# Kernel optimization log

Hardware: AMD Instinct MI355X
Metric: run time of the kernel (lower is better)

Reference implementation:

```python
import jax, jax.numpy as jnp
import numpy as np

B, N, E, P, PH, H = 4, 512, 768, 64, 32, 8
D = E // H  # 96
FFN = 3072

def _ln(x, g, b, eps=1e-5):
    mu = jnp.mean(x, axis=-1, keepdims=True)
    var = jnp.mean((x - mu) ** 2, axis=-1, keepdims=True)
    return (x - mu) * jax.lax.rsqrt(var + eps) * g + b

def setup_inputs() -> dict:
    key = jax.random.key(0)
    ks = iter(jax.random.split(key, 80))
    def f(*s):
        return jax.random.normal(next(ks), s, jnp.float32) * 0.02
    ones = lambda *s: jnp.ones(s, jnp.float32)
    zeros = lambda *s: jnp.zeros(s, jnp.float32)
    return {
        'x': jax.random.normal(next(ks), (B, N, E), jnp.float32),
        'pair': jax.random.normal(next(ks), (B, N, N, P), jnp.float32) * 0.5,
        'attn_mask': zeros(B, 1, N, N),
        'op_mask': ones(B, N, 1),
        'op_norm': ones(1) / N,
        'nlist': jax.random.randint(next(ks), (B, N, 64), 0, N),
        'wq': f(E, E), 'wk': f(E, E), 'wv': f(E, E),
        'wg': f(E, E), 'bg': zeros(E),
        'wo': f(E, E), 'bo': zeros(E),
        'ln_pair_g': ones(P), 'ln_pair_b': zeros(P),
        'wb': f(H, P), 'bb': zeros(H),
        'ln_attn_g': ones(E), 'ln_attn_b': zeros(E),
        'ln_ffn_g': ones(E), 'ln_ffn_b': zeros(E),
        'w_ffn1': f(FFN, E), 'b_ffn1': zeros(FFN),
        'w_ffn2': f(E, FFN), 'b_ffn2': zeros(E),
        'ln_opm_g': ones(E), 'ln_opm_b': zeros(E),
        'w_opm_in': f(2 * PH, E), 'b_opm_in': zeros(2 * PH),
        'w_opm_out': f(P, PH * PH), 'b_opm_out': zeros(P),
        'ln_tm_g': ones(P), 'ln_tm_b': zeros(P),
        'w_tm_abp': f(2 * PH, P), 'b_tm_abp': zeros(2 * PH),
        'w_tm_abg': f(2 * PH, P), 'b_tm_abg': zeros(2 * PH),
        'w_tm_g': f(P, P), 'b_tm_g': zeros(P),
        'w_tm_z': f(P, PH), 'b_tm_z': zeros(P),
        'ln_tmo_g': ones(PH), 'ln_tmo_b': zeros(PH),
        'ln_pffn_g': ones(P), 'ln_pffn_b': zeros(P),
        'w_pffn1': f(P, P), 'b_pffn1': zeros(P),
        'w_pffn2': f(P, P), 'b_pffn2': zeros(P),
    }

def _forward(x, pair, attn_mask, op_mask, op_norm, wq, wk, wv, wg, bg, wo, bo,
             ln_pair_g, ln_pair_b, wb, bb, ln_attn_g, ln_attn_b,
             ln_ffn_g, ln_ffn_b, w_ffn1, b_ffn1, w_ffn2, b_ffn2,
             ln_opm_g, ln_opm_b, w_opm_in, b_opm_in, w_opm_out, b_opm_out,
             ln_tm_g, ln_tm_b, w_tm_abp, b_tm_abp, w_tm_abg, b_tm_abg,
             w_tm_g, b_tm_g, w_tm_z, b_tm_z, ln_tmo_g, ln_tmo_b,
             ln_pffn_g, ln_pffn_b, w_pffn1, b_pffn1, w_pffn2, b_pffn2):
    Bx, Nx, _ = x.shape
    # --- gated pair-bias self-attention (pre-LN, eval mode: dropout = identity) ---
    h = _ln(x, ln_attn_g, ln_attn_b)
    pn = _ln(pair, ln_pair_g, ln_pair_b)               # AtomAttention pair LayerNorm
    bias = jnp.einsum('bijp,hp->bhij', pn, wb) + bb[None, :, None, None]
    q = (h @ wq.T).reshape(Bx, Nx, H, D).transpose(0, 2, 1, 3) * (D ** -0.5)
    k = (h @ wk.T).reshape(Bx, Nx, H, D).transpose(0, 2, 1, 3)
    v = (h @ wv.T).reshape(Bx, Nx, H, D).transpose(0, 2, 1, 3)
    attn = jax.nn.softmax(jnp.einsum('bhid,bhjd->bhij', q, k) + attn_mask + bias, axis=-1)
    o = jnp.einsum('bhij,bhjd->bhid', attn, v).transpose(0, 2, 1, 3).reshape(Bx, Nx, E)
    o = jax.nn.sigmoid(h @ wg.T + bg) * o              # sigmoid output gate
    x = x + (o @ wo.T + bo)
    # --- atom transition MLP ---
    h = _ln(x, ln_ffn_g, ln_ffn_b)
    x = x + (jax.nn.gelu(h @ w_ffn1.T + b_ffn1, approximate=False) @ w_ffn2.T + b_ffn2)
    # --- OuterProduct pair update (fused: avoids [B,N,N,PH*PH] intermediate) ---
    h = _ln(x, ln_opm_g, ln_opm_b)
    ab = (h @ w_opm_in.T + b_opm_in) * op_mask
    a_o, b_o = jnp.split(ab, 2, axis=-1)               # each [B,N,PH]
    z = jnp.einsum('bid,bje,pde->bijp', a_o, b_o, w_opm_out.reshape(P, PH, PH)) + b_opm_out
    pair = pair + z * op_norm
    # --- triangle multiplication ---
    zp = _ln(pair, ln_tm_g, ln_tm_b)
    gpr = zp @ w_tm_g.T + b_tm_g                       # gate (no sigmoid, matches source)
    ab = (zp @ w_tm_abp.T + b_tm_abp) * jax.nn.sigmoid(zp @ w_tm_abg.T + b_tm_abg)
    a_t, b_t = jnp.split(ab, 2, axis=-1)               # each [B,N,N,PH]
    t = jnp.einsum('bijh,bkjh->bhik', a_t, b_t) + jnp.einsum('bjih,bjkh->bhik', a_t, b_t)
    t = _ln(t.transpose(0, 2, 3, 1), ln_tmo_g, ln_tmo_b) @ w_tm_z.T + b_tm_z
    pair = pair + gpr * t
    # --- pair transition MLP ---
    zp = _ln(pair, ln_pffn_g, ln_pffn_b)
    pair = pair + (jax.nn.gelu(zp @ w_pffn1.T + b_pffn1, approximate=False) @ w_pffn2.T + b_pffn2)
    return x, pair

def reference(x, pair, attn_mask, op_mask, op_norm, nlist, wq, wk, wv, wg, bg, wo, bo,
              ln_pair_g, ln_pair_b, wb, bb, ln_attn_g, ln_attn_b,
              ln_ffn_g, ln_ffn_b, w_ffn1, b_ffn1, w_ffn2, b_ffn2,
              ln_opm_g, ln_opm_b, w_opm_in, b_opm_in, w_opm_out, b_opm_out,
              ln_tm_g, ln_tm_b, w_tm_abp, b_tm_abp, w_tm_abg, b_tm_abg,
              w_tm_g, b_tm_g, w_tm_z, b_tm_z, ln_tmo_g, ln_tmo_b,
              ln_pffn_g, ln_pffn_b, w_pffn1, b_pffn1, w_pffn2, b_pffn2):
    del nlist  # accepted by the torch module but unused in the math
    return _forward(x, pair, attn_mask, op_mask, op_norm, wq, wk, wv, wg, bg, wo, bo,
                    ln_pair_g, ln_pair_b, wb, bb, ln_attn_g, ln_attn_b,
                    ln_ffn_g, ln_ffn_b, w_ffn1, b_ffn1, w_ffn2, b_ffn2,
                    ln_opm_g, ln_opm_b, w_opm_in, b_opm_in, w_opm_out, b_opm_out,
                    ln_tm_g, ln_tm_b, w_tm_abp, b_tm_abp, w_tm_abg, b_tm_abg,
                    w_tm_g, b_tm_g, w_tm_z, b_tm_z, ln_tmo_g, ln_tmo_b,
                    ln_pffn_g, ln_pffn_b, w_pffn1, b_pffn1, w_pffn2, b_pffn2)
```

## Files before the change

### kernel.cpp

```cpp
#include <hip/hip_runtime.h>
#include <hip/hip_bf16.h>
#include <math.h>

#define Nn 512
#define Ee 768
#define Pp 64
#define PHh 32
#define Hh 8
#define Dd 96
#define NNe 262144
#define LNEPS 1e-5f

typedef __attribute__((ext_vector_type(8))) short bf8;
typedef __attribute__((ext_vector_type(4))) short bf4;
typedef __attribute__((ext_vector_type(4))) float f32x4;
#define MFMA(a,b,c) __builtin_amdgcn_mfma_f32_16x16x32_bf16(a,b,c,0,0,0)

__device__ __forceinline__ short f2bf(float f) {
  unsigned u = __builtin_bit_cast(unsigned, f);
  unsigned r = (u + 0x7fffu + ((u >> 16) & 1u)) >> 16;
  return (short)r;
}
__device__ __forceinline__ float bf2f(short s) {
  unsigned u = ((unsigned)(unsigned short)s) << 16;
// ... 376 lines not shown
  float rsum[4] = {0.f, 0.f, 0.f, 0.f};
#pragma unroll
  for (int jf = 0; jf < 8; ++jf)
#pragma unroll
    for (int r = 0; r < 4; ++r) {
      float e = __expf(sv[jf][r] - rmax[r]);
      sv[jf][r] = e;
      rsum[r] += e;
    }
#pragma unroll
  for (int r = 0; r < 4; ++r) {
#pragma unroll
    for (int off = 1; off < 16; off <<= 1) rsum[r] += __shfl_xor(rsum[r], off, 16);
    if (llo == 0) redB[wv][lhi * 4 + r] = rsum[r];
  }
  __syncthreads();
#pragma unroll
  for (int r = 0; r < 4; ++r) {
    int row = lhi * 4 + r;
    float s = redB[0][row] + redB[1][row] + redB[2][row] + redB[3][row];
    float inv = 1.f / s;
#pragma unroll
    for (int jf = 0; jf < 8; ++jf) {
      int j = jb0 + jf * 16 + llo;
      out_bf[bioff + (long)row * 512 + j] = f2bf(sv[jf][r] * inv);
    }
  }
}

__global__ __launch_bounds__(256) void opm_T_kernel(const float* __restrict__ ab,
                                                    const float* __restrict__ mask,
                                                    const float* __restrict__ w,
                                                    short* __restrict__ T,
                                                    short* __restrict__ bo_bf) {
  int p = blockIdx.y;
  int row = blockIdx.x * 8 + threadIdx.y;
  int e = threadIdx.x;
  float mk = mask[row];
  const float* a = ab + (long)row * 64;
  const float* wp = w + p * 1024 + e;
  float acc = 0.f;
#pragma unroll
  for (int d = 0; d < 32; ++d) acc += a[d] * wp[d * 32];
  T[((long)row * 64 + p) * 32 + e] = f2bf(acc * mk);
  if (blockIdx.y == 0) bo_bf[(long)row * 32 + e] = f2bf(a[32 + e] * mk);
}

__global__ __launch_bounds__(256) void pair_bias_mfma(
    const float* __restrict__ pair, const float* __restrict__ gam,
    const float* __restrict__ bet, const short* __restrict__ wb_a,
    const float* __restrict__ bbv, short* __restrict__ bias,
    short* __restrict__ pair_bf) {
  __shared__ __align__(16) short Zb[64 * 72];
  __shared__ __align__(16) short Wb[16 * 72];
  __shared__ float sp[4][2][72];
  int tid = threadIdx.x;
  long e0 = (long)blockIdx.x * 64;
  int b = (int)(e0 >> 18);
  long ein = e0 & (NNe - 1);
  const float* base = pair + e0 * 64;
  for (int l = tid; l < 1024; l += 256) {
    int h = l >> 6, c = l & 63;
    Wb[h * 72 + c] = (h < 8) ? wb_a[h * 64 + c] : (short)0;
  }
  int e = tid & 63, q = tid >> 6;
  f32x4 v4[4];
  float s = 0.f, ss = 0.f;
#pragma unroll
  for (int k = 0; k < 4; ++k) {
    v4[k] = *(const f32x4*)(base + (long)e * 64 + q * 16 + k * 4);
#pragma unroll
    for (int u = 0; u < 4; ++u) { float v = v4[k][u]; s += v; ss += v * v; }
  }
#pragma unroll
  for (int k = 0; k < 4; ++k) {
    bf4 pr;
#pragma unroll
    for (int u = 0; u < 4; ++u) pr[u] = f2bf(v4[k][u]);
    *(bf4*)(pair_bf + (e0 + e) * 64 + q * 16 + k * 4) = pr;
  }
  sp[q][0][e] = s; sp[q][1][e] = ss;
  __syncthreads();
  float ts = sp[0][0][e] + sp[1][0][e] + sp[2][0][e] + sp[3][0][e];
  float tss = sp[0][1][e] + sp[1][1][e] + sp[2][1][e] + sp[3][1][e];
  float mu = ts * 0.015625f, var = tss * 0.015625f - mu * mu;
  float rs = rsqrtf(var + LNEPS);
#pragma unroll
  for (int k = 0; k < 4; ++k) {
    bf4 pk;
#pragma unroll
    for (int u = 0; u < 4; ++u) {
      int c = q * 16 + k * 4 + u;
      pk[u] = f2bf((v4[k][u] - mu) * rs * gam[c] + bet[c]);
    }
    *(bf4*)&Zb[e * 72 + q * 16 + k * 4] = pk;
  }
  __syncthreads();
  int wv = tid >> 6, lane = tid & 63;
  int lhi = lane >> 4, llo = lane & 15;
  int n0 = wv * 16;
  f32x4 acc = {0.f, 0.f, 0.f, 0.f};
#pragma unroll
  for (int ks = 0; ks < 2; ++ks) {
    bf8 a = *(const bf8*)&Wb[llo * 72 + ks * 32 + lhi * 8];
    bf8 bz = *(const bf8*)&Zb[(n0 + llo) * 72 + ks * 32 + lhi * 8];
    acc = MFMA(a, bz, acc);
  }
  int elem = n0 + llo;
#pragma unroll
  for (int r = 0; r < 4; ++r) {
    int h = lhi * 4 + r;
    if (h < 8) bias[(long)(b * 8 + h) * NNe + ein + elem] = f2bf(acc[r] + bbv[h]);
  }
}

__global__ __launch_bounds__(256) void opm_ab_fused(
    const short* __restrict__ pair_bf, const short* __restrict__ Tb,
    const short* __restrict__ bo_bf, const float* __restrict__ b_out,
    const float* __restrict__ op_norm, const float* __restrict__ gam,
    const float* __restrict__ bet, const short* __restrict__ wp_a,
    const float* __restrict__ b_abp, const short* __restrict__ wg_a,
    const float* __restrict__ b_abg,
    short* __restrict__ aN4, short* __restrict__ bN4) {
  int jt = blockIdx.x;
  int i = blockIdx.y;
  int bb = blockIdx.z;
  int tid = threadIdx.x;
  __shared__ __align__(16) short Tsb[64 * 40];
  __shared__ __align__(16) short Bob[64 * 40];
  __shared__ __align__(16) short Zb[64 * 72];
  __shared__ __align__(16) short Wp[64 * 72];
  __shared__ __align__(16) short Wg[64 * 72];
  __shared__ float spS[64][9];
  __shared__ float spQ[64][9];
  int wv = tid >> 6, lane = tid & 63;
  int wr = wv >> 1, wc = wv & 1;
  int lhi = lane >> 4, llo = lane & 15;
  int chb = wr * 32 + lhi * 4;
  long grow = (long)bb * 512 + i;
  {
    int p = tid >> 2, e8 = (tid & 3) * 8;
    *(bf8*)&Tsb[p * 40 + e8] = *(const bf8*)(Tb + grow * 2048 + p * 32 + e8);
    *(bf8*)&Bob[p * 40 + e8] =
        *(const bf8*)(bo_bf + ((long)bb * 512 + jt * 64 + p) * 32 + e8);
  }
  for (int l = tid; l < 512; l += 256) {
    int r = l >> 3, c8 = (l & 7) * 8;
    *(bf8*)&Wp[r * 72 + c8] = *(const bf8*)(wp_a + r * 64 + c8);
    *(bf8*)&Wg[r * 72 + c8] = *(const bf8*)(wg_a + r * 64 + c8);
  }
  long ebase = (long)i * 512 + jt * 64;
  const short* pbase = pair_bf + ((long)bb * NNe + ebase) * 64;
  short* aN = aN4 + (long)bb * 8388608;
  short* bN = bN4 + (long)bb * 8388608;
  f32x4 x[2][2];
#pragma unroll
  for (int mi = 0; mi < 2; ++mi)
#pragma unroll
    for (int ni = 0; ni < 2; ++ni) {
      bf4 pv = *(const bf4*)(pbase + (long)(wc * 32 + ni * 16 + llo) * 64 +
                             chb + mi * 16);
#pragma unroll
      for (int r = 0; r < 4; ++r) x[mi][ni][r] = bf2f(pv[r]);
    }
  __syncthreads();
  f32x4 acc[2][2] = {};
  {
    bf8 a0 = *(const bf8*)&Tsb[(wr * 32 + llo) * 40 + lhi * 8];
    bf8 a1 = *(const bf8*)&Tsb[(wr * 32 + 16 + llo) * 40 + lhi * 8];
    bf8 b0 = *(const bf8*)&Bob[(wc * 32 + llo) * 40 + lhi * 8];
    bf8 b1 = *(const bf8*)&Bob[(wc * 32 + 16 + llo) * 40 + lhi * 8];
    acc[0][0] = MFMA(a0, b0, acc[0][0]);
    acc[0][1] = MFMA(a0, b1, acc[0][1]);
    acc[1][0] = MFMA(a1, b0, acc[1][0]);
    acc[1][1] = MFMA(a1, b1, acc[1][1]);
  }
  float nrm = op_norm[0];
#pragma unroll
  for (int mi = 0; mi < 2; ++mi) {
    f32x4 bo4 = *(const f32x4*)(b_out + chb + mi * 16);
#pragma unroll
    for (int ni = 0; ni < 2; ++ni)
#pragma unroll
      for (int r = 0; r < 4; ++r)
        x[mi][ni][r] += (acc[mi][ni][r] + bo4[r]) * nrm;
  }
#pragma unroll
  for (int ni = 0; ni < 2; ++ni) {
    float s = 0.f, ss = 0.f;
#pragma unroll
    for (int mi = 0; mi < 2; ++mi)
#pragma unroll
      for (int r = 0; r < 4; ++r) { float v = x[mi][ni][r]; s += v; ss += v * v; }
    int e = wc * 32 + ni * 16 + llo;
    spS[e][wr * 4 + lhi] = s;
    spQ[e][wr * 4 + lhi] = ss;
  }
  __syncthreads();
  float mu1[2], rs1[2];
#pragma unroll
  for (int ni = 0; ni < 2; ++ni) {
    int e = wc * 32 + ni * 16 + llo;
    float s = 0.f, q2 = 0.f;
#pragma unroll
    for (int k = 0; k < 8; ++k) { s += spS[e][k]; q2 += spQ[e][k]; }
    float mu = s * 0.015625f, var = q2 * 0.015625f - mu * mu;
    mu1[ni] = mu; rs1[ni] = rsqrtf(var + LNEPS);
  }
#pragma unroll
  for (int mi = 0; mi < 2; ++mi) {
    f32x4 gv = *(const f32x4*)(gam + chb + mi * 16);
    f32x4 bv = *(const f32x4*)(bet + chb + mi * 16);
#pragma unroll
    for (int ni = 0; ni < 2; ++ni) {
      int e = wc * 32 + ni * 16 + llo;
      bf4 pk;
#pragma unroll
      for (int r = 0; r < 4; ++r)
        pk[r] = f2bf((x[mi][ni][r] - mu1[ni]) * rs1[ni] * gv[r] + bv[r]);
      *(bf4*)&Zb[e * 72 + chb + mi * 16] = pk;
    }
  }
  __syncthreads();
  f32x4 ap[2][2] = {};
  f32x4 ag[2][2] = {};
#pragma unroll
  for (int ks = 0; ks < 2; ++ks) {
    bf8 z0 = *(const bf8*)&Zb[(wr * 32 + llo) * 72 + ks * 32 + lhi * 8];
    bf8 z1 = *(const bf8*)&Zb[(wr * 32 + 16 + llo) * 72 + ks * 32 + lhi * 8];
    bf8 p0 = *(const bf8*)&Wp[(wc * 32 + llo) * 72 + ks * 32 + lhi * 8];
    bf8 p1 = *(const bf8*)&Wp[(wc * 32 + 16 + llo) * 72 + ks * 32 + lhi * 8];
    bf8 g0 = *(const bf8*)&Wg[(wc * 32 + llo) * 72 + ks * 32 + lhi * 8];
    bf8 g1 = *(const bf8*)&Wg[(wc * 32 + 16 + llo) * 72 + ks * 32 + lhi * 8];
    ap[0][0] = MFMA(z0, p0, ap[0][0]);
    ap[0][1] = MFMA(z0, p1, ap[0][1]);
    ap[1][0] = MFMA(z1, p0, ap[1][0]);
    ap[1][1] = MFMA(z1, p1, ap[1][1]);
    ag[0][0] = MFMA(z0, g0, ag[0][0]);
    ag[0][1] = MFMA(z0, g1, ag[0][1]);
    ag[1][0] = MFMA(z1, g0, ag[1][0]);
    ag[1][1] = MFMA(z1, g1, ag[1][1]);
  }
#pragma unroll
  for (int mi = 0; mi < 2; ++mi) {
    int elemb = wr * 32 + mi * 16 + lhi * 4;
#pragma unroll
    for (int ni = 0; ni < 2; ++ni) {
      int ch = wc * 32 + ni * 16 + llo;
      float bp = b_abp[ch], bg = b_abg[ch];
      bf4 pack;
#pragma unroll
      for (int r = 0; r < 4; ++r)
        pack[r] = f2bf((ap[mi][ni][r] + bp) * sigmoidf_(ag[mi][ni][r] + bg));
      short* dst = (ch < 32) ? (aN + (long)ch * NNe) : (bN + (long)(ch - 32) * NNe);
      *(bf4*)(dst + ebase + elemb) = pack;
    }
  }
}

__global__ __launch_bounds__(512) void tm_tri_mfma(const short* __restrict__ aN4,
                                                   const short* __restrict__ bN4,
                                                   short* __restrict__ t4) {
  int lin = blockIdx.z * 16 + blockIdx.y * 4 + blockIdx.x;
  int vid = (lin & 7) * 256 + (lin >> 3);
  int hh = vid >> 4;
  int b = hh >> 5, h = hh & 31;
  int rem = vid & 15;
  int i0 = (rem >> 2) * 128, k0 = (rem & 3) * 128;
  const short* A = aN4 + (long)b * 8388608 + (long)h * NNe;
  const short* B = bN4 + (long)b * 8388608 + (long)h * NNe;
  __shared__ __align__(16) short A1[128 * 40];
  __shared__ __align__(16) short B1[128 * 40];
  __shared__ __align__(16) short A2[128 * 40];
  __shared__ __align__(16) short B2[128 * 40];
  int tid = threadIdx.x;
  int wv = tid >> 6, lane = tid & 63;
  int wr = wv >> 2, wc = wv & 3;
  int lhi = lane >> 4, llo = lane & 15;
  int r1 = tid >> 2, cp = (tid & 3) * 8;
  int s2 = tid >> 5, cg = (tid & 31) * 4;
  f32x4 acc[4][2] = {};
  for (int j0 = 0; j0 < 512; j0 += 32) {
    *(bf8*)&A1[r1 * 40 + cp] = *(const bf8*)(A + (long)(i0 + r1) * 512 + j0 + cp);
    *(bf8*)&B1[r1 * 40 + cp] = *(const bf8*)(B + (long)(k0 + r1) * 512 + j0 + cp);
    bf4 va0 = *(const bf4*)(A + (long)(j0 + 2 * s2) * 512 + i0 + cg);
    bf4 va1 = *(const bf4*)(A + (long)(j0 + 2 * s2 + 1) * 512 + i0 + cg);
// ... 5 lines not shown
                    ((unsigned)(unsigned short)va1[q] << 16);
      unsigned pb = (unsigned)(unsigned short)vb0[q] |
                    ((unsigned)(unsigned short)vb1[q] << 16);
      *(unsigned*)&A2[(cg + q) * 40 + 2 * s2] = pa;
      *(unsigned*)&B2[(cg + q) * 40 + 2 * s2] = pb;
    }
    __syncthreads();
    bf8 bfr[2], dfr[2];
#pragma unroll
    for (int ni = 0; ni < 2; ++ni) {
      bfr[ni] = *(const bf8*)&B1[(wc * 32 + ni * 16 + llo) * 40 + lhi * 8];
      dfr[ni] = *(const bf8*)&B2[(wc * 32 + ni * 16 + llo) * 40 + lhi * 8];
    }
#pragma unroll
    for (int mi = 0; mi < 4; ++mi) {
      bf8 a = *(const bf8*)&A1[(wr * 64 + mi * 16 + llo) * 40 + lhi * 8];
      acc[mi][0] = MFMA(a, bfr[0], acc[mi][0]);
      acc[mi][1] = MFMA(a, bfr[1], acc[mi][1]);
    }
#pragma unroll
    for (int mi = 0; mi < 4; ++mi) {
      bf8 c = *(const bf8*)&A2[(wr * 64 + mi * 16 + llo) * 40 + lhi * 8];
      acc[mi][0] = MFMA(c, dfr[0], acc[mi][0]);
      acc[mi][1] = MFMA(c, dfr[1], acc[mi][1]);
    }
    __syncthreads();
  }
  short* tp = t4 + (long)b * 8388608 + (long)h * NNe;
#pragma unroll
  for (int mi = 0; mi < 4; ++mi)
#pragma unroll
    for (int ni = 0; ni < 2; ++ni) {
      int row = i0 + wr * 64 + mi * 16 + lhi * 4;
      int col = k0 + wc * 32 + ni * 16 + llo;
#pragma unroll
      for (int r = 0; r < 4; ++r) tp[(long)(row + r) * 512 + col] = f2bf(acc[mi][ni][r]);
    }
}

__global__ __launch_bounds__(256) void upd_pffn_fused(
    const short* __restrict__ pair_bf, float* __restrict__ pout,
    const short* __restrict__ t4,
    const short* __restrict__ Tb, const short* __restrict__ bo_bf,
    const float* __restrict__ b_out, const float* __restrict__ op_norm,
    const float* __restrict__ g_tm, const float* __restrict__ b_tm,
    const short* __restrict__ wg_a, const float* __restrict__ b_g,
    const short* __restrict__ wz_a, const float* __restrict__ b_z,
    const float* __restrict__ g_tmo, const float* __restrict__ b_tmo,
    const float* __restrict__ g_pf, const float* __restrict__ b_pf,
    const short* __restrict__ w1_a, const float* __restrict__ b1,
    const short* __restrict__ w2_a, const float* __restrict__ b2) {
  __shared__ __align__(16) short Zb[64 * 72];
  __shared__ __align__(16) short Tlb[64 * 40];
  __shared__ __align__(16) short Wbuf[64 * 72];
  __shared__ __align__(16) short Wzb[64 * 40];
  __shared__ __align__(16) short Tsb[64 * 40];
  __shared__ __align__(16) short Bob[64 * 40];
  __shared__ float spS[64][9];
  __shared__ float spQ[64][9];
  __shared__ float spB[4][2][72];
  int tid = threadIdx.x;
  long e0 = (long)blockIdx.x * 64;
  int bbt = (int)(e0 >> 18);
  long el = e0 & (NNe - 1);
  long growT = e0 >> 9;
  int jt = (int)((e0 >> 6) & 7);
  int wv = tid >> 6, lane = tid & 63;
  int wr = wv >> 1, wc = wv & 1;
  int lhi = lane >> 4, llo = lane & 15;
  int chb = wr * 32 + lhi * 4;
  int r0 = tid >> 3, c0 = (tid & 7) * 8;
  int r1 = (tid + 256) >> 3, c1 = ((tid + 256) & 7) * 8;
  bf8 w1r0, w1r1, w2r0, w2r1;
  {
    *(bf8*)&Wbuf[r0 * 72 + c0] = *(const bf8*)(wg_a + r0 * 64 + c0);
    *(bf8*)&Wbuf[r1 * 72 + c1] = *(const bf8*)(wg_a + r1 * 64 + c1);
    w1r0 = *(const bf8*)(w1_a + r0 * 64 + c0);
    w1r1 = *(const bf8*)(w1_a + r1 * 64 + c1);
    w2r0 = *(const bf8*)(w2_a + r0 * 64 + c0);
    w2r1 = *(const bf8*)(w2_a + r1 * 64 + c1);
    int rz = tid >> 2, cz = (tid & 3) * 8;
    *(bf8*)&Wzb[rz * 40 + cz] = *(const bf8*)(wz_a + rz * 32 + cz);
    int p = tid >> 2, e8 = (tid & 3) * 8;
    *(bf8*)&Tsb[p * 40 + e8] = *(const bf8*)(Tb + growT * 2048 + p * 32 + e8);
    *(bf8*)&Bob[p * 40 + e8] =
        *(const bf8*)(bo_bf + ((long)bbt * 512 + jt * 64 + p) * 32 + e8);
  }
  f32x4 x[2][2];
#pragma unroll
  for (int mi = 0; mi < 2; ++mi)
#pragma unroll
    for (int ni = 0; ni < 2; ++ni) {
      bf4 pv = *(const bf4*)(pair_bf + (e0 + wc * 32 + ni * 16 + llo) * 64 +
                             chb + mi * 16);
#pragma unroll
      for (int r = 0; r < 4; ++r) x[mi][ni][r] = bf2f(pv[r]);
    }
  const short* t_in = t4 + (long)bbt * 8388608;
  int te = tid & 63, tq = tid >> 6;
  float tt[8];
  {
    float sB = 0.f, ssB = 0.f;
#pragma unroll
    for (int k = 0; k < 8; ++k) {
      float v = bf2f(t_in[(long)(tq * 8 + k) * NNe + el + te]);
      tt[k] = v; sB += v; ssB += v * v;
    }
    spB[tq][0][te] = sB; spB[tq][1][te] = ssB;
  }
  __syncthreads();
  {
    float ts = spB[0][0][te] + spB[1][0][te] + spB[2][0][te] + spB[3][0][te];
    float tss = spB[0][1][te] + spB[1][1][te] + spB[2][1][te] + spB[3][1][te];
    float mu = ts * 0.03125f, var = tss * 0.03125f - mu * mu;
    float rs = rsqrtf(var + LNEPS);
    bf8 pk;
#pragma unroll
    for (int k = 0; k < 8; ++k) {
      int c = tq * 8 + k;
      pk[k] = f2bf((tt[k] - mu) * rs * g_tmo[c] + b_tmo[c]);
    }
    *(bf8*)&Tlb[te * 40 + tq * 8] = pk;
  }
  {
    f32x4 acc[2][2] = {};
    bf8 a0 = *(const bf8*)&Tsb[(wr * 32 + llo) * 40 + lhi * 8];
    bf8 a1 = *(const bf8*)&Tsb[(wr * 32 + 16 + llo) * 40 + lhi * 8];
    bf8 b0 = *(const bf8*)&Bob[(wc * 32 + llo) * 40 + lhi * 8];
    bf8 b1 = *(const bf8*)&Bob[(wc * 32 + 16 + llo) * 40 + lhi * 8];
    acc[0][0] = MFMA(a0, b0, acc[0][0]);
    acc[0][1] = MFMA(a0, b1, acc[0][1]);
    acc[1][0] = MFMA(a1, b0, acc[1][0]);
    acc[1][1] = MFMA(a1, b1, acc[1][1]);
    float nrm = op_norm[0];
#pragma unroll
    for (int mi = 0; mi < 2; ++mi) {
      f32x4 bo4 = *(const f32x4*)(b_out + chb + mi * 16);
#pragma unroll
      for (int ni = 0; ni < 2; ++ni)
#pragma unroll
        for (int r = 0; r < 4; ++r)
          x[mi][ni][r] += (acc[mi][ni][r] + bo4[r]) * nrm;
    }
  }
#pragma unroll
  for (int ni = 0; ni < 2; ++ni) {
    float s = 0.f, ss = 0.f;
#pragma unroll
    for (int mi = 0; mi < 2; ++mi)
#pragma unroll
      for (int r = 0; r < 4; ++r) { float v = x[mi][ni][r]; s += v; ss += v * v; }
    int e = wc * 32 + ni * 16 + llo;
    spS[e][wr * 4 + lhi] = s;
    spQ[e][wr * 4 + lhi] = ss;
  }
  __syncthreads();
  float mu1[2], rs1[2];
#pragma unroll
  for (int ni = 0; ni < 2; ++ni) {
    int e = wc * 32 + ni * 16 + llo;
    float s = 0.f, q2 = 0.f;
#pragma unroll
    for (int k = 0; k < 8; ++k) { s += spS[e][k]; q2 += spQ[e][k]; }
    float mu = s * 0.015625f, var = q2 * 0.015625f - mu * mu;
    mu1[ni] = mu; rs1[ni] = rsqrtf(var + LNEPS);
  }
#pragma unroll
  for (int mi = 0; mi < 2; ++mi) {
    f32x4 gv = *(const f32x4*)(g_tm + chb + mi * 16);
    f32x4 bv = *(const f32x4*)(b_tm + chb + mi * 16);
#pragma unroll
    for (int ni = 0; ni < 2; ++ni) {
      int e = wc * 32 + ni * 16 + llo;
      bf4 pk;
#pragma unroll
      for (int r = 0; r < 4; ++r)
        pk[r] = f2bf((x[mi][ni][r] - mu1[ni]) * rs1[ni] * gv[r] + bv[r]);
      *(bf4*)&Zb[e * 72 + chb + mi * 16] = pk;
    }
  }
  __syncthreads();
  f32x4 accg[2][2] = {};
  f32x4 accz[2][2] = {};
#pragma unroll
  for (int ks = 0; ks < 2; ++ks) {
    bf8 a0 = *(const bf8*)&Wbuf[(wr * 32 + llo) * 72 + ks * 32 + lhi * 8];
    bf8 a1 = *(const bf8*)&Wbuf[(wr * 32 + 16 + llo) * 72 + ks * 32 + lhi * 8];
    bf8 z0 = *(const bf8*)&Zb[(wc * 32 + llo) * 72 + ks * 32 + lhi * 8];
    bf8 z1 = *(const bf8*)&Zb[(wc * 32 + 16 + llo) * 72 + ks * 32 + lhi * 8];
    accg[0][0] = MFMA(a0, z0, accg[0][0]);
    accg[0][1] = MFMA(a0, z1, accg[0][1]);
    accg[1][0] = MFMA(a1, z0, accg[1][0]);
    accg[1][1] = MFMA(a1, z1, accg[1][1]);
  }
  {
    bf8 a0 = *(const bf8*)&Wzb[(wr * 32 + llo) * 40 + lhi * 8];
    bf8 a1 = *(const bf8*)&Wzb[(wr * 32 + 16 + llo) * 40 + lhi * 8];
    bf8 t0 = *(const bf8*)&Tlb[(wc * 32 + llo) * 40 + lhi * 8];
    bf8 t1 = *(const bf8*)&Tlb[(wc * 32 + 16 + llo) * 40 + lhi * 8];
    accz[0][0] = MFMA(a0, t0, accz[0][0]);
    accz[0][1] = MFMA(a0, t1, accz[0][1]);
    accz[1][0] = MFMA(a1, t0, accz[1][0]);
    accz[1][1] = MFMA(a1, t1, accz[1][1]);
  }
#pragma unroll
  for (int mi = 0; mi < 2; ++mi) {
    f32x4 bgv = *(const f32x4*)(b_g + chb + mi * 16);
    f32x4 bzv = *(const f32x4*)(b_z + chb + mi * 16);
#pragma unroll
    for (int ni = 0; ni < 2; ++ni)
#pragma unroll
      for (int r = 0; r < 4; ++r)
        x[mi][ni][r] += (accg[mi][ni][r] + bgv[r]) * (accz[mi][ni][r] + bzv[r]);
  }
#pragma unroll
  for (int ni = 0; ni < 2; ++ni) {
    float s = 0.f, ss = 0.f;
#pragma unroll
    for (int mi = 0; mi < 2; ++mi)
#pragma unroll
      for (int r = 0; r < 4; ++r) { float v = x[mi][ni][r]; s += v; ss += v * v; }
    int e = wc * 32 + ni * 16 + llo;
    spS[e][wr * 4 + lhi] = s;
    spQ[e][wr * 4 + lhi] = ss;
  }
  __syncthreads();
  *(bf8*)&Wbuf[r0 * 72 + c0] = w1r0;
  *(bf8*)&Wbuf[r1 * 72 + c1] = w1r1;
#pragma unroll
  for (int ni = 0; ni < 2; ++ni) {
    int e = wc * 32 + ni * 16 + llo;
    float s = 0.f, q2 = 0.f;
#pragma unroll
    for (int k = 0; k < 8; ++k) { s += spS[e][k]; q2 += spQ[e][k]; }
    float mu = s * 0.015625f, var = q2 * 0.015625f - mu * mu;
    mu1[ni] = mu; rs1[ni] = rsqrtf(var + LNEPS);
  }
#pragma unroll
  for (int mi = 0; mi < 2; ++mi) {
    f32x4 gv = *(const f32x4*)(g_pf + chb + mi * 16);
    f32x4 bv = *(const f32x4*)(b_pf + chb + mi * 16);
#pragma unroll
    for (int ni = 0; ni < 2; ++ni) {
      int e = wc * 32 + ni * 16 + llo;
      bf4 pk;
#pragma unroll
      for (int r = 0; r < 4; ++r)
        pk[r] = f2bf((x[mi][ni][r] - mu1[ni]) * rs1[ni] * gv[r] + bv[r]);
      *(bf4*)&Zb[e * 72 + chb + mi * 16] = pk;
    }
  }
  __syncthreads();
  f32x4 acc1[2][2] = {};
#pragma unroll
  for (int ks = 0; ks < 2; ++ks) {
    bf8 a0 = *(const bf8*)&Wbuf[(wr * 32 + llo) * 72 + ks * 32 + lhi * 8];
    bf8 a1 = *(const bf8*)&Wbuf[(wr * 32 + 16 + llo) * 72 + ks * 32 + lhi * 8];
    bf8 z0 = *(const bf8*)&Zb[(wc * 32 + llo) * 72 + ks * 32 + lhi * 8];
    bf8 z1 = *(const bf8*)&Zb[(wc * 32 + 16 + llo) * 72 + ks * 32 + lhi * 8];
    acc1[0][0] = MFMA(a0, z0, acc1[0][0]);
    acc1[0][1] = MFMA(a0, z1, acc1[0][1]);
    acc1[1][0] = MFMA(a1, z0, acc1[1][0]);
    acc1[1][1] = MFMA(a1, z1, acc1[1][1]);
  }
  __syncthreads();
  *(bf8*)&Wbuf[r0 * 72 + c0] = w2r0;
  *(bf8*)&Wbuf[r1 * 72 + c1] = w2r1;
#pragma unroll
  for (int mi = 0; mi < 2; ++mi) {
    f32x4 bv = *(const f32x4*)(b1 + chb + mi * 16);
#pragma unroll
    for (int ni = 0; ni < 2; ++ni) {
      int e = wc * 32 + ni * 16 + llo;
      bf4 pk;
#pragma unroll
      for (int r = 0; r < 4; ++r) pk[r] = f2bf(gelu_exact(acc1[mi][ni][r] + bv[r]));
      *(bf4*)&Zb[e * 72 + chb + mi * 16] = pk;
    }
  }
  __syncthreads();
  f32x4 acc2[2][2] = {};
#pragma unroll
  for (int ks = 0; ks < 2; ++ks) {
    bf8 a0 = *(const bf8*)&Wbuf[(wr * 32 + llo) * 72 + ks * 32 + lhi * 8];
    bf8 a1 = *(const bf8*)&Wbuf[(wr * 32 + 16 + llo) * 72 + ks * 32 + lhi * 8];
    bf8 z0 = *(const bf8*)&Zb[(wc * 32 + llo) * 72 + ks * 32 + lhi * 8];
    bf8 z1 = *(const bf8*)&Zb[(wc * 32 + 16 + llo) * 72 + ks * 32 + lhi * 8];
    acc2[0][0] = MFMA(a0, z0, acc2[0][0]);
    acc2[0][1] = MFMA(a0, z1, acc2[0][1]);
    acc2[1][0] = MFMA(a1, z0, acc2[1][0]);
    acc2[1][1] = MFMA(a1, z1, acc2[1][1]);
  }
#pragma unroll
  for (int mi = 0; mi < 2; ++mi) {
    f32x4 bv = *(const f32x4*)(b2 + chb + mi * 16);
#pragma unroll
    for (int ni = 0; ni < 2; ++ni) {
#pragma unroll
      for (int r = 0; r < 4; ++r) x[mi][ni][r] += acc2[mi][ni][r] + bv[r];
      *(f32x4*)(pout + (e0 + wc * 32 + ni * 16 + llo) * 64 + chb + mi * 16) =
          x[mi][ni];
    }
  }
}

extern "C" void kernel_launch(void* const* d_in, const int* in_sizes, int n_in,
                              void* d_out, int out_size, void* d_ws, size_t ws_size,
                              hipStream_t stream) {
  const float* x = (const float*)d_in[0];
  const float* pair = (const float*)d_in[1];
  const float* attn_mask = (const float*)d_in[2];
  const float* op_mask = (const float*)d_in[3];
  const float* op_norm = (const float*)d_in[4];
  const float* wq = (const float*)d_in[6];
  const float* wk = (const float*)d_in[7];
  const float* wv_ = (const float*)d_in[8];
  const float* wg = (const float*)d_in[9];
  const float* bg = (const float*)d_in[10];
  const float* wo = (const float*)d_in[11];
  const float* bo = (const float*)d_in[12];
  const float* ln_pair_g = (const float*)d_in[13];
  const float* ln_pair_b = (const float*)d_in[14];
  const float* wb = (const float*)d_in[15];
  const float* bb = (const float*)d_in[16];
  const float* ln_attn_g = (const float*)d_in[17];
  const float* ln_attn_b = (const float*)d_in[18];
  const float* ln_ffn_g = (const float*)d_in[19];
  const float* ln_ffn_b = (const float*)d_in[20];
  const float* w_ffn1 = (const float*)d_in[21];
  const float* b_ffn1 = (const float*)d_in[22];
  const float* w_ffn2 = (const float*)d_in[23];
  const float* b_ffn2 = (const float*)d_in[24];
  const float* ln_opm_g = (const float*)d_in[25];
  const float* ln_opm_b = (const float*)d_in[26];
  const float* w_opm_in = (const float*)d_in[27];
  const float* b_opm_in = (const float*)d_in[28];
  const float* w_opm_out = (const float*)d_in[29];
  const float* b_opm_out = (const float*)d_in[30];
  const float* ln_tm_g = (const float*)d_in[31];
  const float* ln_tm_b = (const float*)d_in[32];
// ... 26 lines not shown
  short* wabg_a = wbf + 7721472;
  short* wtg_a = wbf + 7725568;
  short* wtz_a = wbf + 7729664;
  short* wp1_a = wbf + 7731712;
  short* wp2_a = wbf + 7735808;

  short* h_bf = (short*)(ws + 3869952);
  short* q_bf = (short*)(ws + 4656384);
  short* k_bf = (short*)(ws + 5442816);
  short* vT_bf = (short*)(ws + 6229248);
  float* gb = ws + 7015680;
  short* gb_bf = (short*)(ws + 10161408);
  float* x1b = ws + 10947840;
  short* biasb_bf = (short*)(ws + 12520704);
  short* attn_bf = (short*)(ws + 16715008);
  short* mffn_bf = (short*)(ws + 20909312);
  float* abb = ws + 24055040;
  short* bo_bf = (short*)(ws + 24186112);
  short* Tb_bf = (short*)(ws + 24218880);
  short* pair_bfp = (short*)(ws + 26316032);
  short* aN4 = (short*)(ws + 59870464);
  short* bN4 = (short*)(ws + 76647680);
  short* t4 = (short*)(ws + 93424896);

  float* xo = (float*)d_out;
  float* pair1 = xo + 1572864;

  const float qscale = 0.1020620726159658f;

  castw_kernel<<<30234, 256, 0, stream>>>(wq, wk, wv_, wg, wo, w_ffn1, w_ffn2, w_opm_in,
                                          wb, w_tm_abp, w_tm_abg, w_tm_g, w_tm_z,
                                          w_pffn1, w_pffn2, wbf, qscale);
  ln_bf_kernel<<<2048, 256, 0, stream>>>(x, h_bf, ln_attn_g, ln_attn_b, 768);
  gemm_qkvg<<<dim3(24, 16, 1), 256, 0, stream>>>(h_bf, wq_bf, q_bf, k_bf, vT_bf, gb, bg);
  pair_bias_mfma<<<16384, 256, 0, stream>>>(pair, ln_pair_g, ln_pair_b, wb_a, bb,
                                            biasb_bf, pair_bfp);
  attn_fused<<<dim3(32, 8, 4), 256, 0, stream>>>(q_bf, k_bf, biasb_bf, attn_mask, attn_bf);
  gemm_bf<<<dim3(2, 8, 32), 256, 0, stream>>>(attn_bf, 512, 2097152, 262144,
                                              vT_bf, 512, 393216, 49152,
                                              nullptr, 0, 393216, 96, gb_bf, 768,
                                              gb, 768, 393216, 96, nullptr,
                                              512, 96, 512, 2, 0, 8);
  gemm128<<<dim3(6, 16, 1), 256, 0, stream>>>(gb_bf, wo_bf, 768, x, bo, x1b);
  ln_bf_kernel<<<2048, 256, 0, stream>>>(x1b, h_bf, ln_ffn_g, ln_ffn_b, 768);
  gemm_ffn1<<<dim3(24, 16, 1), 256, 0, stream>>>(h_bf, wf1_bf, mffn_bf, b_ffn1);
  gemm128<<<dim3(6, 16, 1), 256, 0, stream>>>(mffn_bf, wf2_bf, 3072, x1b, b_ffn2, xo);
  ln_bf_kernel<<<2048, 256, 0, stream>>>(xo, h_bf, ln_opm_g, ln_opm_b, 768);
  gemm_bf<<<dim3(1, 32, 1), 256, 0, stream>>>(h_bf, 768, 0, 0, wop_bf, 768, 0, 0,
                                              abb, 64, 0, 0, nullptr, 0,
                                              nullptr, 0, 0, 0, b_opm_in,
                                              2048, 64, 768, 0, 0, 1);
  opm_T_kernel<<<dim3(256, 64, 1), dim3(32, 8, 1), 0, stream>>>(abb, op_mask, w_opm_out,
                                                                Tb_bf, bo_bf);
  opm_ab_fused<<<dim3(8, 512, 4), 256, 0, stream>>>(
      pair_bfp, Tb_bf, bo_bf, b_opm_out, op_norm,
      ln_tm_g, ln_tm_b, wabp_a, b_tm_abp, wabg_a, b_tm_abg, aN4, bN4);
  tm_tri_mfma<<<dim3(4, 4, 128), 512, 0, stream>>>(aN4, bN4, t4);
  upd_pffn_fused<<<16384, 256, 0, stream>>>(
      pair_bfp, pair1, t4, Tb_bf, bo_bf, b_opm_out, op_norm,
      ln_tm_g, ln_tm_b, wtg_a, b_tm_g, wtz_a, b_tm_z,
      ln_tmo_g, ln_tmo_b, ln_pffn_g, ln_pffn_b, wp1_a, b_pffn1, wp2_a, b_pffn2);
}
```

Baseline: 940.5 us.

## Load small weights and OPM factors directly from global instead of LDS staging

In the pair bias, OPM/triangle-input and pair-update/FFN kernels, the weight matrices and the per-row OPM factors are now read straight from global memory into MFMA fragments instead of being staged through shared memory. This removes LDS stores, shrinks the shared-memory footprint and removes a synchronisation point. The pair-update kernel is reordered so the OPM and triangle layernorm work overlaps the t4 load, and both fused kernels use a 1D grid with a remapped block index to change the order in which blocks run. The cost is more global and cache traffic for weights that every block fetches again.

Measured after the change: 989.2 us. 1.05x slower.

```diff
diff --git a/kernel.cpp b/kernel.cpp
--- a/kernel.cpp
+++ b/kernel.cpp
@@ -452,17 +452,12 @@
     const float* __restrict__ bbv, short* __restrict__ bias,
     short* __restrict__ pair_bf) {
   __shared__ __align__(16) short Zb[64 * 72];
-  __shared__ __align__(16) short Wb[16 * 72];
   __shared__ float sp[4][2][72];
   int tid = threadIdx.x;
   long e0 = (long)blockIdx.x * 64;
   int b = (int)(e0 >> 18);
   long ein = e0 & (NNe - 1);
   const float* base = pair + e0 * 64;
-  for (int l = tid; l < 1024; l += 256) {
-    int h = l >> 6, c = l & 63;
-    Wb[h * 72 + c] = (h < 8) ? wb_a[h * 64 + c] : (short)0;
-  }
   int e = tid & 63, q = tid >> 6;
   f32x4 v4[4];
   float s = 0.f, ss = 0.f;
@@ -502,7 +497,8 @@
   f32x4 acc = {0.f, 0.f, 0.f, 0.f};
 #pragma unroll
   for (int ks = 0; ks < 2; ++ks) {
-    bf8 a = *(const bf8*)&Wb[llo * 72 + ks * 32 + lhi * 8];
+    bf8 a = {};
+    if (llo < 8) a = *(const bf8*)(wb_a + llo * 64 + ks * 32 + lhi * 8);
     bf8 bz = *(const bf8*)&Zb[(n0 + llo) * 72 + ks * 32 + lhi * 8];
     acc = MFMA(a, bz, acc);
   }
@@ -522,33 +518,21 @@
     const float* __restrict__ b_abp, const short* __restrict__ wg_a,
     const float* __restrict__ b_abg,
     short* __restrict__ aN4, short* __restrict__ bN4) {
-  int jt = blockIdx.x;
-  int i = blockIdx.y;
-  int bb = blockIdx.z;
-  int tid = threadIdx.x;
-  __shared__ __align__(16) short Tsb[64 * 40];
-  __shared__ __align__(16) short Bob[64 * 40];
   __shared__ __align__(16) short Zb[64 * 72];
-  __shared__ __align__(16) short Wp[64 * 72];
-  __shared__ __align__(16) short Wg[64 * 72];
   __shared__ float spS[64][9];
   __shared__ float spQ[64][9];
+  int tid = threadIdx.x;
+  int lin = blockIdx.x;
+  int vid = (lin & 7) * 2048 + (lin >> 3);
+  int bb = vid >> 12;
+  int i = (vid >> 3) & 511;
+  int jt = vid & 7;
   int wv = tid >> 6, lane = tid & 63;
   int wr = wv >> 1, wc = wv & 1;
   int lhi = lane >> 4, llo = lane & 15;
   int chb = wr * 32 + lhi * 4;
+  int fc = lhi * 8;
   long grow = (long)bb * 512 + i;
-  {
-    int p = tid >> 2, e8 = (tid & 3) * 8;
-    *(bf8*)&Tsb[p * 40 + e8] = *(const bf8*)(Tb + grow * 2048 + p * 32 + e8);
-    *(bf8*)&Bob[p * 40 + e8] =
-        *(const bf8*)(bo_bf + ((long)bb * 512 + jt * 64 + p) * 32 + e8);
-  }
-  for (int l = tid; l < 512; l += 256) {
-    int r = l >> 3, c8 = (l & 7) * 8;
-    *(bf8*)&Wp[r * 72 + c8] = *(const bf8*)(wp_a + r * 64 + c8);
-    *(bf8*)&Wg[r * 72 + c8] = *(const bf8*)(wg_a + r * 64 + c8);
-  }
   long ebase = (long)i * 512 + jt * 64;
   const short* pbase = pair_bf + ((long)bb * NNe + ebase) * 64;
   short* aN = aN4 + (long)bb * 8388608;
@@ -563,27 +547,27 @@
 #pragma unroll
       for (int r = 0; r < 4; ++r) x[mi][ni][r] = bf2f(pv[r]);
     }
-  __syncthreads();
-  f32x4 acc[2][2] = {};
   {
-    bf8 a0 = *(const bf8*)&Tsb[(wr * 32 + llo) * 40 + lhi * 8];
-    bf8 a1 = *(const bf8*)&Tsb[(wr * 32 + 16 + llo) * 40 + lhi * 8];
-    bf8 b0 = *(const bf8*)&Bob[(wc * 32 + llo) * 40 + lhi * 8];
-    bf8 b1 = *(const bf8*)&Bob[(wc * 32 + 16 + llo) * 40 + lhi * 8];
+    f32x4 acc[2][2] = {};
+    bf8 a0 = *(const bf8*)(Tb + grow * 2048 + (long)(wr * 32 + llo) * 32 + fc);
+    bf8 a1 = *(const bf8*)(Tb + grow * 2048 + (long)(wr * 32 + 16 + llo) * 32 + fc);
+    bf8 b0 = *(const bf8*)(bo_bf + ((long)bb * 512 + jt * 64 + wc * 32 + llo) * 32 + fc);
+    bf8 b1 = *(const bf8*)(bo_bf +
+                           ((long)bb * 512 + jt * 64 + wc * 32 + 16 + llo) * 32 + fc);
     acc[0][0] = MFMA(a0, b0, acc[0][0]);
     acc[0][1] = MFMA(a0, b1, acc[0][1]);
     acc[1][0] = MFMA(a1, b0, acc[1][0]);
     acc[1][1] = MFMA(a1, b1, acc[1][1]);
-  }
-  float nrm = op_norm[0];
-#pragma unroll
-  for (int mi = 0; mi < 2; ++mi) {
-    f32x4 bo4 = *(const f32x4*)(b_out + chb + mi * 16);
-#pragma unroll
-    for (int ni = 0; ni < 2; ++ni)
-#pragma unroll
-      for (int r = 0; r < 4; ++r)
-        x[mi][ni][r] += (acc[mi][ni][r] + bo4[r]) * nrm;
+    float nrm = op_norm[0];
+#pragma unroll
+    for (int mi = 0; mi < 2; ++mi) {
+      f32x4 bo4 = *(const f32x4*)(b_out + chb + mi * 16);
+#pragma unroll
+      for (int ni = 0; ni < 2; ++ni)
+#pragma unroll
+        for (int r = 0; r < 4; ++r)
+          x[mi][ni][r] += (acc[mi][ni][r] + bo4[r]) * nrm;
+    }
   }
 #pragma unroll
   for (int ni = 0; ni < 2; ++ni) {
@@ -626,12 +610,12 @@
   f32x4 ag[2][2] = {};
 #pragma unroll
   for (int ks = 0; ks < 2; ++ks) {
-    bf8 z0 = *(const bf8*)&Zb[(wr * 32 + llo) * 72 + ks * 32 + lhi * 8];
-    bf8 z1 = *(const bf8*)&Zb[(wr * 32 + 16 + llo) * 72 + ks * 32 + lhi * 8];
-    bf8 p0 = *(const bf8*)&Wp[(wc * 32 + llo) * 72 + ks * 32 + lhi * 8];
-    bf8 p1 = *(const bf8*)&Wp[(wc * 32 + 16 + llo) * 72 + ks * 32 + lhi * 8];
-    bf8 g0 = *(const bf8*)&Wg[(wc * 32 + llo) * 72 + ks * 32 + lhi * 8];
-    bf8 g1 = *(const bf8*)&Wg[(wc * 32 + 16 + llo) * 72 + ks * 32 + lhi * 8];
+    bf8 z0 = *(const bf8*)&Zb[(wr * 32 + llo) * 72 + ks * 32 + fc];
+    bf8 z1 = *(const bf8*)&Zb[(wr * 32 + 16 + llo) * 72 + ks * 32 + fc];
+    bf8 p0 = *(const bf8*)(wp_a + (long)(wc * 32 + llo) * 64 + ks * 32 + fc);
+    bf8 p1 = *(const bf8*)(wp_a + (long)(wc * 32 + 16 + llo) * 64 + ks * 32 + fc);
+    bf8 g0 = *(const bf8*)(wg_a + (long)(wc * 32 + llo) * 64 + ks * 32 + fc);
+    bf8 g1 = *(const bf8*)(wg_a + (long)(wc * 32 + 16 + llo) * 64 + ks * 32 + fc);
     ap[0][0] = MFMA(z0, p0, ap[0][0]);
     ap[0][1] = MFMA(z0, p1, ap[0][1]);
     ap[1][0] = MFMA(z1, p0, ap[1][0]);
@@ -743,15 +727,13 @@
     const short* __restrict__ w2_a, const float* __restrict__ b2) {
   __shared__ __align__(16) short Zb[64 * 72];
   __shared__ __align__(16) short Tlb[64 * 40];
-  __shared__ __align__(16) short Wbuf[64 * 72];
-  __shared__ __align__(16) short Wzb[64 * 40];
-  __shared__ __align__(16) short Tsb[64 * 40];
-  __shared__ __align__(16) short Bob[64 * 40];
   __shared__ float spS[64][9];
   __shared__ float spQ[64][9];
   __shared__ float spB[4][2][72];
   int tid = threadIdx.x;
-  long e0 = (long)blockIdx.x * 64;
+  int lin = blockIdx.x;
+  int vid = (lin & 7) * 2048 + (lin >> 3);
+  long e0 = (long)vid * 64;
   int bbt = (int)(e0 >> 18);
   long el = e0 & (NNe - 1);
   long growT = e0 >> 9;
@@ -760,23 +742,9 @@
   int wr = wv >> 1, wc = wv & 1;
   int lhi = lane >> 4, llo = lane & 15;
   int chb = wr * 32 + lhi * 4;
-  int r0 = tid >> 3, c0 = (tid & 7) * 8;
-  int r1 = (tid + 256) >> 3, c1 = ((tid + 256) & 7) * 8;
-  bf8 w1r0, w1r1, w2r0, w2r1;
-  {
-    *(bf8*)&Wbuf[r0 * 72 + c0] = *(const bf8*)(wg_a + r0 * 64 + c0);
-    *(bf8*)&Wbuf[r1 * 72 + c1] = *(const bf8*)(wg_a + r1 * 64 + c1);
-    w1r0 = *(const bf8*)(w1_a + r0 * 64 + c0);
-    w1r1 = *(const bf8*)(w1_a + r1 * 64 + c1);
-    w2r0 = *(const bf8*)(w2_a + r0 * 64 + c0);
-    w2r1 = *(const bf8*)(w2_a + r1 * 64 + c1);
-    int rz = tid >> 2, cz = (tid & 3) * 8;
-    *(bf8*)&Wzb[rz * 40 + cz] = *(const bf8*)(wz_a + rz * 32 + cz);
-    int p = tid >> 2, e8 = (tid & 3) * 8;
-    *(bf8*)&Tsb[p * 40 + e8] = *(const bf8*)(Tb + growT * 2048 + p * 32 + e8);
-    *(bf8*)&Bob[p * 40 + e8] =
-        *(const bf8*)(bo_bf + ((long)bbt * 512 + jt * 64 + p) * 32 + e8);
-  }
+  int fc = lhi * 8;
+  int fr0 = wr * 32 + llo, fr1 = fr0 + 16;
+  int br0 = wc * 32 + llo, br1 = br0 + 16;
   f32x4 x[2][2];
 #pragma unroll
   for (int mi = 0; mi < 2; ++mi)
@@ -787,6 +755,38 @@
 #pragma unroll
       for (int r = 0; r < 4; ++r) x[mi][ni][r] = bf2f(pv[r]);
     }
+  {
+    f32x4 acc[2][2] = {};
+    bf8 a0 = *(const bf8*)(Tb + growT * 2048 + (long)fr0 * 32 + fc);
+    bf8 a1 = *(const bf8*)(Tb + growT * 2048 + (long)fr1 * 32 + fc);
+    bf8 b0 = *(const bf8*)(bo_bf + ((long)bbt * 512 + jt * 64 + br0) * 32 + fc);
+    bf8 b1 = *(const bf8*)(bo_bf + ((long)bbt * 512 + jt * 64 + br1) * 32 + fc);
+    acc[0][0] = MFMA(a0, b0, acc[0][0]);
+    acc[0][1] = MFMA(a0, b1, acc[0][1]);
+    acc[1][0] = MFMA(a1, b0, acc[1][0]);
+    acc[1][1] = MFMA(a1, b1, acc[1][1]);
+    float nrm = op_norm[0];
+#pragma unroll
+    for (int mi = 0; mi < 2; ++mi) {
+      f32x4 bo4 = *(const f32x4*)(b_out + chb + mi * 16);
+#pragma unroll
+      for (int ni = 0; ni < 2; ++ni)
+#pragma unroll
+        for (int r = 0; r < 4; ++r)
+          x[mi][ni][r] += (acc[mi][ni][r] + bo4[r]) * nrm;
+    }
+  }
+#pragma unroll
+  for (int ni = 0; ni < 2; ++ni) {
+    float s = 0.f, ss = 0.f;
+#pragma unroll
+    for (int mi = 0; mi < 2; ++mi)
+#pragma unroll
+      for (int r = 0; r < 4; ++r) { float v = x[mi][ni][r]; s += v; ss += v * v; }
+    int e = wc * 32 + ni * 16 + llo;
+    spS[e][wr * 4 + lhi] = s;
+    spQ[e][wr * 4 + lhi] = ss;
+  }
   const short* t_in = t4 + (long)bbt * 8388608;
   int te = tid & 63, tq = tid >> 6;
   float tt[8];
@@ -813,26 +813,63 @@
     }
     *(bf8*)&Tlb[te * 40 + tq * 8] = pk;
   }
+  float mu1[2], rs1[2];
+#pragma unroll
+  for (int ni = 0; ni < 2; ++ni) {
+    int e = wc * 32 + ni * 16 + llo;
+    float s = 0.f, q2 = 0.f;
+#pragma unroll
+    for (int k = 0; k < 8; ++k) { s += spS[e][k]; q2 += spQ[e][k]; }
+    float mu = s * 0.015625f, var = q2 * 0.015625f - mu * mu;
+    mu1[ni] = mu; rs1[ni] = rsqrtf(var + LNEPS);
+  }
+#pragma unroll
+  for (int mi = 0; mi < 2; ++mi) {
+    f32x4 gv = *(const f32x4*)(g_tm + chb + mi * 16);
+    f32x4 bv = *(const f32x4*)(b_tm + chb + mi * 16);
+#pragma unroll
+    for (int ni = 0; ni < 2; ++ni) {
+      int e = wc * 32 + ni * 16 + llo;
+      bf4 pk;
+#pragma unroll
+      for (int r = 0; r < 4; ++r)
+        pk[r] = f2bf((x[mi][ni][r] - mu1[ni]) * rs1[ni] * gv[r] + bv[r]);
+      *(bf4*)&Zb[e * 72 + chb + mi * 16] = pk;
+    }
+  }
+  __syncthreads();
+  f32x4 accg[2][2] = {};
+  f32x4 accz[2][2] = {};
+#pragma unroll
+  for (int ks = 0; ks < 2; ++ks) {
+    bf8 a0 = *(const bf8*)(wg_a + (long)fr0 * 64 + ks * 32 + fc);
+    bf8 a1 = *(const bf8*)(wg_a + (long)fr1 * 64 + ks * 32 + fc);
+    bf8 z0 = *(const bf8*)&Zb[br0 * 72 + ks * 32 + fc];
+    bf8 z1 = *(const bf8*)&Zb[br1 * 72 + ks * 32 + fc];
+    accg[0][0] = MFMA(a0, z0, accg[0][0]);
+    accg[0][1] = MFMA(a0, z1, accg[0][1]);
+    accg[1][0] = MFMA(a1, z0, accg[1][0]);
+    accg[1][1] = MFMA(a1, z1, accg[1][1]);
+  }
   {
-    f32x4 acc[2][2] = {};
-    bf8 a0 = *(const bf8*)&Tsb[(wr * 32 + llo) * 40 + lhi * 8];
-    bf8 a1 = *(const bf8*)&Tsb[(wr * 32 + 16 + llo) * 40 + lhi * 8];
-    bf8 b0 = *(const bf8*)&Bob[(wc * 32 + llo) * 40 + lhi * 8];
-    bf8 b1 = *(const bf8*)&Bob[(wc * 32 + 16 + llo) * 40 + lhi * 8];
-    acc[0][0] = MFMA(a0, b0, acc[0][0]);
-    acc[0][1] = MFMA(a0, b1, acc[0][1]);
-    acc[1][0] = MFMA(a1, b0, acc[1][0]);
-    acc[1][1] = MFMA(a1, b1, acc[1][1]);
-    float nrm = op_norm[0];
-#pragma unroll
-    for (int mi = 0; mi < 2; ++mi) {
-      f32x4 bo4 = *(const f32x4*)(b_out + chb + mi * 16);
-#pragma unroll
-      for (int ni = 0; ni < 2; ++ni)
-#pragma unroll
-        for (int r = 0; r < 4; ++r)
-          x[mi][ni][r] += (acc[mi][ni][r] + bo4[r]) * nrm;
-    }
+    bf8 a0 = *(const bf8*)(wz_a + (long)fr0 * 32 + fc);
+    bf8 a1 = *(const bf8*)(wz_a + (long)fr1 * 32 + fc);
+    bf8 t0 = *(const bf8*)&Tlb[br0 * 40 + fc];
+    bf8 t1 = *(const bf8*)&Tlb[br1 * 40 + fc];
+    accz[0][0] = MFMA(a0, t0, accz[0][0]);
+    accz[0][1] = MFMA(a0, t1, accz[0][1]);
+    accz[1][0] = MFMA(a1, t0, accz[1][0]);
+    accz[1][1] = MFMA(a1, t1, accz[1][1]);
+  }
+#pragma unroll
+  for (int mi = 0; mi < 2; ++mi) {
+    f32x4 bgv = *(const f32x4*)(b_g + chb + mi * 16);
+    f32x4 bzv = *(const f32x4*)(b_z + chb + mi * 16);
+#pragma unroll
+    for (int ni = 0; ni < 2; ++ni)
+#pragma unroll
+      for (int r = 0; r < 4; ++r)
+        x[mi][ni][r] += (accg[mi][ni][r] + bgv[r]) * (accz[mi][ni][r] + bzv[r]);
   }
 #pragma unroll
   for (int ni = 0; ni < 2; ++ni) {
@@ -846,7 +883,6 @@
     spQ[e][wr * 4 + lhi] = ss;
   }
   __syncthreads();
-  float mu1[2], rs1[2];
 #pragma unroll
   for (int ni = 0; ni < 2; ++ni) {
     int e = wc * 32 + ni * 16 + llo;
@@ -858,8 +894,8 @@
   }
 #pragma unroll
   for (int mi = 0; mi < 2; ++mi) {
-    f32x4 gv = *(const f32x4*)(g_tm + chb + mi * 16);
-    f32x4 bv = *(const f32x4*)(b_tm + chb + mi * 16);
+    f32x4 gv = *(const f32x4*)(g_pf + chb + mi * 16);
+    f32x4 bv = *(const f32x4*)(b_pf + chb + mi * 16);
 #pragma unroll
     for (int ni = 0; ni < 2; ++ni) {
       int e = wc * 32 + ni * 16 + llo;
@@ -871,92 +907,19 @@
     }
   }
   __syncthreads();
-  f32x4 accg[2][2] = {};
-  f32x4 accz[2][2] = {};
+  f32x4 acc1[2][2] = {};
 #pragma unroll
   for (int ks = 0; ks < 2; ++ks) {
-    bf8 a0 = *(const bf8*)&Wbuf[(wr * 32 + llo) * 72 + ks * 32 + lhi * 8];
-    bf8 a1 = *(const bf8*)&Wbuf[(wr * 32 + 16 + llo) * 72 + ks * 32 + lhi * 8];
-    bf8 z0 = *(const bf8*)&Zb[(wc * 32 + llo) * 72 + ks * 32 + lhi * 8];
-    bf8 z1 = *(const bf8*)&Zb[(wc * 32 + 16 + llo) * 72 + ks * 32 + lhi * 8];
-    accg[0][0] = MFMA(a0, z0, accg[0][0]);
-    accg[0][1] = MFMA(a0, z1, accg[0][1]);
-    accg[1][0] = MFMA(a1, z0, accg[1][0]);
-    accg[1][1] = MFMA(a1, z1, accg[1][1]);
-  }
-  {
-    bf8 a0 = *(const bf8*)&Wzb[(wr * 32 + llo) * 40 + lhi * 8];
-    bf8 a1 = *(const bf8*)&Wzb[(wr * 32 + 16 + llo) * 40 + lhi * 8];
-    bf8 t0 = *(const bf8*)&Tlb[(wc * 32 + llo) * 40 + lhi * 8];
-    bf8 t1 = *(const bf8*)&Tlb[(wc * 32 + 16 + llo) * 40 + lhi * 8];
-    accz[0][0] = MFMA(a0, t0, accz[0][0]);
-    accz[0][1] = MFMA(a0, t1, accz[0][1]);
-    accz[1][0] = MFMA(a1, t0, accz[1][0]);
-    accz[1][1] = MFMA(a1, t1, accz[1][1]);
-  }
-#pragma unroll
-  for (int mi = 0; mi < 2; ++mi) {
-    f32x4 bgv = *(const f32x4*)(b_g + chb + mi * 16);
-    f32x4 bzv = *(const f32x4*)(b_z + chb + mi * 16);
-#pragma unroll
-    for (int ni = 0; ni < 2; ++ni)
-#pragma unroll
-      for (int r = 0; r < 4; ++r)
-        x[mi][ni][r] += (accg[mi][ni][r] + bgv[r]) * (accz[mi][ni][r] + bzv[r]);
-  }
-#pragma unroll
-  for (int ni = 0; ni < 2; ++ni) {
-    float s = 0.f, ss = 0.f;
-#pragma unroll
-    for (int mi = 0; mi < 2; ++mi)
-#pragma unroll
-      for (int r = 0; r < 4; ++r) { float v = x[mi][ni][r]; s += v; ss += v * v; }
-    int e = wc * 32 + ni * 16 + llo;
-    spS[e][wr * 4 + lhi] = s;
-    spQ[e][wr * 4 + lhi] = ss;
-  }
-  __syncthreads();
-  *(bf8*)&Wbuf[r0 * 72 + c0] = w1r0;
-  *(bf8*)&Wbuf[r1 * 72 + c1] = w1r1;
-#pragma unroll
-  for (int ni = 0; ni < 2; ++ni) {
-    int e = wc * 32 + ni * 16 + llo;
-    float s = 0.f, q2 = 0.f;
-#pragma unroll
-    for (int k = 0; k < 8; ++k) { s += spS[e][k]; q2 += spQ[e][k]; }
-    float mu = s * 0.015625f, var = q2 * 0.015625f - mu * mu;
-    mu1[ni] = mu; rs1[ni] = rsqrtf(var + LNEPS);
-  }
-#pragma unroll
-  for (int mi = 0; mi < 2; ++mi) {
-    f32x4 gv = *(const f32x4*)(g_pf + chb + mi * 16);
-    f32x4 bv = *(const f32x4*)(b_pf + chb + mi * 16);
-#pragma unroll
-    for (int ni = 0; ni < 2; ++ni) {
-      int e = wc * 32 + ni * 16 + llo;
-      bf4 pk;
-#pragma unroll
-      for (int r = 0; r < 4; ++r)
-        pk[r] = f2bf((x[mi][ni][r] - mu1[ni]) * rs1[ni] * gv[r] + bv[r]);
-      *(bf4*)&Zb[e * 72 + chb + mi * 16] = pk;
-    }
-  }
-  __syncthreads();
-  f32x4 acc1[2][2] = {};
-#pragma unroll
-  for (int ks = 0; ks < 2; ++ks) {
-    bf8 a0 = *(const bf8*)&Wbuf[(wr * 32 + llo) * 72 + ks * 32 + lhi * 8];
-    bf8 a1 = *(const bf8*)&Wbuf[(wr * 32 + 16 + llo) * 72 + ks * 32 + lhi * 8];
-    bf8 z0 = *(const bf8*)&Zb[(wc * 32 + llo) * 72 + ks * 32 + lhi * 8];
-    bf8 z1 = *(const bf8*)&Zb[(wc * 32 + 16 + llo) * 72 + ks * 32 + lhi * 8];
+    bf8 a0 = *(const bf8*)(w1_a + (long)fr0 * 64 + ks * 32 + fc);
+    bf8 a1 = *(const bf8*)(w1_a + (long)fr1 * 64 + ks * 32 + fc);
+    bf8 z0 = *(const bf8*)&Zb[br0 * 72 + ks * 32 + fc];
+    bf8 z1 = *(const bf8*)&Zb[br1 * 72 + ks * 32 + fc];
     acc1[0][0] = MFMA(a0, z0, acc1[0][0]);
     acc1[0][1] = MFMA(a0, z1, acc1[0][1]);
     acc1[1][0] = MFMA(a1, z0, acc1[1][0]);
     acc1[1][1] = MFMA(a1, z1, acc1[1][1]);
   }
   __syncthreads();
-  *(bf8*)&Wbuf[r0 * 72 + c0] = w2r0;
-  *(bf8*)&Wbuf[r1 * 72 + c1] = w2r1;
 #pragma unroll
   for (int mi = 0; mi < 2; ++mi) {
     f32x4 bv = *(const f32x4*)(b1 + chb + mi * 16);
@@ -973,10 +936,10 @@
   f32x4 acc2[2][2] = {};
 #pragma unroll
   for (int ks = 0; ks < 2; ++ks) {
-    bf8 a0 = *(const bf8*)&Wbuf[(wr * 32 + llo) * 72 + ks * 32 + lhi * 8];
-    bf8 a1 = *(const bf8*)&Wbuf[(wr * 32 + 16 + llo) * 72 + ks * 32 + lhi * 8];
-    bf8 z0 = *(const bf8*)&Zb[(wc * 32 + llo) * 72 + ks * 32 + lhi * 8];
-    bf8 z1 = *(const bf8*)&Zb[(wc * 32 + 16 + llo) * 72 + ks * 32 + lhi * 8];
+    bf8 a0 = *(const bf8*)(w2_a + (long)fr0 * 64 + ks * 32 + fc);
+    bf8 a1 = *(const bf8*)(w2_a + (long)fr1 * 64 + ks * 32 + fc);
+    bf8 z0 = *(const bf8*)&Zb[br0 * 72 + ks * 32 + fc];
+    bf8 z1 = *(const bf8*)&Zb[br1 * 72 + ks * 32 + fc];
     acc2[0][0] = MFMA(a0, z0, acc2[0][0]);
     acc2[0][1] = MFMA(a0, z1, acc2[0][1]);
     acc2[1][0] = MFMA(a1, z0, acc2[1][0]);
@@ -1109,7 +1072,7 @@
                                               2048, 64, 768, 0, 0, 1);
   opm_T_kernel<<<dim3(256, 64, 1), dim3(32, 8, 1), 0, stream>>>(abb, op_mask, w_opm_out,
                                                                 Tb_bf, bo_bf);
-  opm_ab_fused<<<dim3(8, 512, 4), 256, 0, stream>>>(
+  opm_ab_fused<<<16384, 256, 0, stream>>>(
       pair_bfp, Tb_bf, bo_bf, b_opm_out, op_norm,
       ln_tm_g, ln_tm_b, wabp_a, b_tm_abp, wabg_a, b_tm_abg, aN4, bN4);
   tm_tri_mfma<<<dim3(4, 4, 128), 512, 0, stream>>>(aN4, bN4, t4);
```
